# Optimization experiments

Hardware: AMD Instinct MI355X
Metric: run time of the kernel (lower is better)

## Reference

```python
import jax, jax.numpy as jnp
import numpy as np

WINDOW_SIZE = 256

def setup_inputs() -> dict:
    key = jax.random.key(0)
    kq, kk, kv = jax.random.split(key, 3)
    B, H, S, D = 1, 16, 4096, 64
    return {
        "query": jax.random.normal(kq, (B, H, S, D), dtype=jnp.float32),
        "key": jax.random.normal(kk, (B, H, S, D), dtype=jnp.float32),
        "value": jax.random.normal(kv, (B, H, S, D), dtype=jnp.float32),
    }

def reference(query, key, value):
    # Faithful to the torch module: dense QK^T, banded mask with -1e9 fill,
    # softmax over full row, then AV. Returns (output, attention_weights).
    d_k = query.shape[-1]
    S = query.shape[2]
    scores = jnp.einsum("bhqd,bhkd->bhqk", query, key) / jnp.sqrt(jnp.float32(d_k))
    idx = jnp.arange(S)
    band = jnp.abs(idx[:, None] - idx[None, :]) <= WINDOW_SIZE  # [S, S]
    scores = jnp.where(band[None, None, :, :], scores, jnp.float32(-1e9))
    attn = jax.nn.softmax(scores, axis=-1)
    out = jnp.einsum("bhqk,bhkd->bhqd", attn, value)
    return (out, attn)
```

## Files before the change

### kernel.cpp

```cpp
#include <hip/hip_runtime.h>
#include <math.h>

#define S_LEN 4096
#define D_DIM 64
#define H_NUM 16
#define WIN   256
#define TQ    32
#define NCH   9
#define KSTR  72
#define PBSTR 584

typedef __attribute__((ext_vector_type(8))) short          bf16x8;
typedef __attribute__((ext_vector_type(4))) float          f32x4;
typedef __attribute__((ext_vector_type(8))) unsigned short u16x8;
typedef __attribute__((ext_vector_type(4))) unsigned short u16x4;

static __device__ __forceinline__ unsigned short f2bf(float x) {
    unsigned int u = __float_as_uint(x);
    u = (u + 0x7FFFu + ((u >> 16) & 1u)) >> 16;
    return (unsigned short)u;
}
static __device__ __forceinline__ float bf2f(unsigned short h) {
    return __uint_as_float(((unsigned int)h) << 16);
}

__global__ __launch_bounds__(256) void swa_kernel(
    const float* __restrict__ Q,
    const float* __restrict__ K,
    const float* __restrict__ V,
    float* __restrict__ out,
    float* __restrict__ attn)
{
    const int tid = threadIdx.x;
    const int q0  = blockIdx.x * TQ;
    const int h   = blockIdx.y;

    const float* __restrict__ Qh = Q + (size_t)h * S_LEN * D_DIM;
    const float* __restrict__ Kh = K + (size_t)h * S_LEN * D_DIM;
    const float* __restrict__ Vh = V + (size_t)h * S_LEN * D_DIM;

    __shared__ unsigned short qbf[TQ * KSTR];
    __shared__ unsigned short kvb[64 * KSTR];
    __shared__ unsigned short pbf[TQ * PBSTR];
    __shared__ float red[4 * TQ];
    __shared__ float linv[TQ];

    const int k0   = max(q0 - WIN, 0);
    const int lane = tid & 63;
    const int wv   = tid >> 6;
    const int quad = lane >> 4;
    const int n16  = lane & 15;

    const int skey = tid >> 2, sd0 = (tid & 3) * 16;

    float4 kx0, kx1, kx2, kx3;
    {
        const int kg = min(k0 + skey, S_LEN - 1);
        const float4* s4 = (const float4*)(Kh + (size_t)kg * D_DIM + sd0);
        kx0 = s4[0]; kx1 = s4[1]; kx2 = s4[2]; kx3 = s4[3];
    }

    {
        const int row = tid >> 3, c8 = (tid & 7) * 8;
        const float4 v0 = *(const float4*)(Qh + (size_t)(q0 + row) * D_DIM + c8);
        const float4 v1 = *(const float4*)(Qh + (size_t)(q0 + row) * D_DIM + c8 + 4);
        u16x8 p;
        p[0]=f2bf(v0.x); p[1]=f2bf(v0.y); p[2]=f2bf(v0.z); p[3]=f2bf(v0.w);
        p[4]=f2bf(v1.x); p[5]=f2bf(v1.y); p[6]=f2bf(v1.z); p[7]=f2bf(v1.w);
        *(u16x8*)&qbf[row * KSTR + c8] = p;
    }
    __syncthreads();

    bf16x8 aqf[2][2];
    #pragma unroll
    for (int qt = 0; qt < 2; ++qt) {
        aqf[qt][0] = *(const bf16x8*)&qbf[(qt * 16 + n16) * KSTR + quad * 8];
        aqf[qt][1] = *(const bf16x8*)&qbf[(qt * 16 + n16) * KSTR + 32 + quad * 8];
    }

    float psum[8] = {0.f,0.f,0.f,0.f,0.f,0.f,0.f,0.f};
    #pragma unroll
    for (int c = 0; c < NCH; ++c) {
        const int kb = k0 + c * 64;
        {
            u16x8 p0, p1;
            p0[0]=f2bf(kx0.x); p0[1]=f2bf(kx0.y); p0[2]=f2bf(kx0.z); p0[3]=f2bf(kx0.w);
            p0[4]=f2bf(kx1.x); p0[5]=f2bf(kx1.y); p0[6]=f2bf(kx1.z); p0[7]=f2bf(kx1.w);
            p1[0]=f2bf(kx2.x); p1[1]=f2bf(kx2.y); p1[2]=f2bf(kx2.z); p1[3]=f2bf(kx2.w);
            p1[4]=f2bf(kx3.x); p1[5]=f2bf(kx3.y); p1[6]=f2bf(kx3.z); p1[7]=f2bf(kx3.w);
            *(u16x8*)&kvb[skey * KSTR + sd0]     = p0;
            *(u16x8*)&kvb[skey * KSTR + sd0 + 8] = p1;
        }
        __syncthreads();

        if (c + 1 < NCH) {
            const int kg = min(kb + 64 + skey, S_LEN - 1);
            const float4* s4 = (const float4*)(Kh + (size_t)kg * D_DIM + sd0);
            kx0 = s4[0]; kx1 = s4[1]; kx2 = s4[2]; kx3 = s4[3];
        }

        const bf16x8 b0 = *(const bf16x8*)&kvb[(wv * 16 + n16) * KSTR + quad * 8];
        const bf16x8 b1 = *(const bf16x8*)&kvb[(wv * 16 + n16) * KSTR + 32 + quad * 8];
        const int key_abs = kb + wv * 16 + n16;
        #pragma unroll
        for (int qt = 0; qt < 2; ++qt) {
            f32x4 acc = {0.f, 0.f, 0.f, 0.f};
            acc = __builtin_amdgcn_mfma_f32_16x16x32_bf16(aqf[qt][0], b0, acc, 0, 0, 0);
            acc = __builtin_amdgcn_mfma_f32_16x16x32_bf16(aqf[qt][1], b1, acc, 0, 0, 0);

            #pragma unroll
            for (int r = 0; r < 4; ++r) {
                const int qrow  = qt * 16 + quad * 4 + r;
                const int q_abs = q0 + qrow;
                const bool in   = (key_abs < S_LEN) &&
                                  (key_abs >= q_abs - WIN) && (key_abs <= q_abs + WIN);
                const float e = in ? __expf(acc[r] * 0.125f) : 0.f;
                pbf[qrow * PBSTR + c * 64 + wv * 16 + n16] = f2bf(e);
                psum[qt * 4 + r] += e;
            }
        }
        __syncthreads();
    }

    float4 vx0, vx1, vx2, vx3;
    {
        const int kg = min(k0 + skey, S_LEN - 1);
        const float4* s4 = (const float4*)(Vh + (size_t)kg * D_DIM + sd0);
        vx0 = s4[0]; vx1 = s4[1]; vx2 = s4[2]; vx3 = s4[3];
    }

    #pragma unroll
    for (int i = 0; i < 8; ++i) {
        float s = psum[i];
        s += __shfl_down(s, 8, 16);
        s += __shfl_down(s, 4, 16);
        s += __shfl_down(s, 2, 16);
        s += __shfl_down(s, 1, 16);
        if (n16 == 0) red[wv * TQ + (i >> 2) * 16 + quad * 4 + (i & 3)] = s;
    }
    __syncthreads();
    if (tid < TQ)
        linv[tid] = 1.f / (red[tid] + red[TQ + tid] + red[2 * TQ + tid] + red[3 * TQ + tid]);
    __syncthreads();

    f32x4 oacc0 = {0.f, 0.f, 0.f, 0.f};
    f32x4 oacc1 = {0.f, 0.f, 0.f, 0.f};
    const int dd = wv * 16 + n16;
    const int sd = ((dd >> 4) + (dd & 7)) & 7;
    #pragma unroll
    for (int c = 0; c < NCH; ++c) {
        {
            const float vals[16] = {vx0.x,vx0.y,vx0.z,vx0.w, vx1.x,vx1.y,vx1.z,vx1.w,
                                    vx2.x,vx2.y,vx2.z,vx2.w, vx3.x,vx3.y,vx3.z,vx3.w};
            #pragma unroll
            for (int jj = 0; jj < 16; ++jj) {
                const int d  = sd0 + jj;
                const int sw = ((d >> 4) + (d & 7)) & 7;
                kvb[d * 64 + (skey ^ (sw * 8))] = f2bf(vals[jj]);
            }
        }
        __syncthreads();

        if (c + 1 < NCH) {
            const int kg = min(k0 + (c + 1) * 64 + skey, S_LEN - 1);
            const float4* s4 = (const float4*)(Vh + (size_t)kg * D_DIM + sd0);
            vx0 = s4[0]; vx1 = s4[1]; vx2 = s4[2]; vx3 = s4[3];
        }

        const bf16x8 vb0 = *(const bf16x8*)&kvb[dd * 64 + 8 * (quad ^ sd)];
        const bf16x8 vb1 = *(const bf16x8*)&kvb[dd * 64 + 8 * ((4 + quad) ^ sd)];
        const bf16x8 pa00 = *(const bf16x8*)&pbf[n16 * PBSTR + c * 64 + quad * 8];
        const bf16x8 pa01 = *(const bf16x8*)&pbf[n16 * PBSTR + c * 64 + 32 + quad * 8];
        const bf16x8 pa10 = *(const bf16x8*)&pbf[(16 + n16) * PBSTR + c * 64 + quad * 8];
        const bf16x8 pa11 = *(const bf16x8*)&pbf[(16 + n16) * PBSTR + c * 64 + 32 + quad * 8];
        oacc0 = __builtin_amdgcn_mfma_f32_16x16x32_bf16(pa00, vb0, oacc0, 0, 0, 0);
        oacc0 = __builtin_amdgcn_mfma_f32_16x16x32_bf16(pa01, vb1, oacc0, 0, 0, 0);
        oacc1 = __builtin_amdgcn_mfma_f32_16x16x32_bf16(pa10, vb0, oacc1, 0, 0, 0);
        oacc1 = __builtin_amdgcn_mfma_f32_16x16x32_bf16(pa11, vb1, oacc1, 0, 0, 0);
        __syncthreads();
    }
    #pragma unroll
    for (int r = 0; r < 4; ++r) {
        const int qr = quad * 4 + r;
        out[((size_t)h * S_LEN + q0 + qr) * D_DIM + dd]      = oacc0[r] * linv[qr];
        out[((size_t)h * S_LEN + q0 + 16 + qr) * D_DIM + dd] = oacc1[r] * linv[16 + qr];
    }

    for (int qq = 0; qq < TQ; ++qq) {
        const int qa  = q0 + qq;
        const int b0q = max(qa - WIN, 0);
        const int b1q = min(qa + WIN, S_LEN - 1);
        const float qi = linv[qq];
        f32x4* arow = (f32x4*)(attn + ((size_t)h * S_LEN + qa) * S_LEN);
        const unsigned short* prow = &pbf[qq * PBSTR];
        for (int j4 = tid; j4 < S_LEN / 4; j4 += 256) {
            const int j = j4 * 4;
            f32x4 w = {0.f, 0.f, 0.f, 0.f};
            if (j >= b0q && j + 3 <= b1q) {
                const u16x4 p = *(const u16x4*)&prow[j - k0];
                w[0] = bf2f(p.x) * qi; w[1] = bf2f(p.y) * qi;
                w[2] = bf2f(p.z) * qi; w[3] = bf2f(p.w) * qi;
            } else if (j + 3 >= b0q && j <= b1q) {
                #pragma unroll
                for (int e = 0; e < 4; ++e) {
                    const int jj = j + e;
                    if (jj >= b0q && jj <= b1q) w[e] = bf2f(prow[jj - k0]) * qi;
                }
            }
            __builtin_nontemporal_store(w, &arow[j4]);
        }
    }
}

extern "C" void kernel_launch(void* const* d_in, const int* in_sizes, int n_in,
                              void* d_out, int out_size, void* d_ws, size_t ws_size,
                              hipStream_t stream) {
    const float* Q = (const float*)d_in[0];
    const float* K = (const float*)d_in[1];
    const float* V = (const float*)d_in[2];
    float* out  = (float*)d_out;
    float* attn = out + (size_t)H_NUM * S_LEN * D_DIM;

    dim3 grid(S_LEN / TQ, H_NUM);
    swa_kernel<<<grid, 256, 0, stream>>>(Q, K, V, out, attn);
}
```

Measured before the change: 1.126 ms.

## Interleave out-of-band attn zero stores with compute phases, write band region at end

The zero fill of the attention matrix outside each block's key window is now spread across the QK and PV chunk loops, two query rows per chunk, so the large store traffic overlaps MFMA and load work. The final epilogue writes only the 144 float4 columns covering the window, instead of sweeping all 4096 columns per row. This keeps the write-bandwidth-bound output streaming through the whole kernel rather than only at the tail, at the cost of extra instructions and register pressure inside the main loops.

```diff
diff --git a/kernel.cpp b/kernel.cpp
--- a/kernel.cpp
+++ b/kernel.cpp
@@ -51,6 +51,29 @@
     const int quad = lane >> 4;
     const int n16  = lane & 15;
 
+    const int l4  = k0 >> 2;
+    const int e4  = l4 + 144;
+    const int r4  = (e4 < 1024) ? (1024 - e4) : 0;
+    const int zp4 = l4 + r4;
+    const f32x4 zero4 = {0.f, 0.f, 0.f, 0.f};
+
+#define ZEROS(p)                                                                 \
+    if ((p) < 16) {                                                              \
+        _Pragma("unroll")                                                        \
+        for (int rr = 0; rr < 2; ++rr) {                                         \
+            const int qq = 2 * (p) + rr;                                         \
+            f32x4* arow = (f32x4*)(attn + ((size_t)h * S_LEN + q0 + qq) * S_LEN);\
+            _Pragma("unroll")                                                    \
+            for (int it = 0; it < 4; ++it) {                                     \
+                const int c4 = tid + it * 256;                                   \
+                if (c4 < zp4) {                                                  \
+                    const int col4 = (c4 < l4) ? c4 : (c4 - l4 + e4);            \
+                    __builtin_nontemporal_store(zero4, &arow[col4]);             \
+                }                                                                \
+            }                                                                    \
+        }                                                                        \
+    }
+
     const int skey = tid >> 2, sd0 = (tid & 3) * 16;
 
     float4 kx0, kx1, kx2, kx3;
@@ -93,6 +116,8 @@
         }
         __syncthreads();
 
+        ZEROS(c);
+
         if (c + 1 < NCH) {
             const int kg = min(kb + 64 + skey, S_LEN - 1);
             const float4* s4 = (const float4*)(Kh + (size_t)kg * D_DIM + sd0);
@@ -161,6 +186,8 @@
         }
         __syncthreads();
 
+        ZEROS(9 + c);
+
         if (c + 1 < NCH) {
             const int kg = min(k0 + (c + 1) * 64 + skey, S_LEN - 1);
             const float4* s4 = (const float4*)(Vh + (size_t)kg * D_DIM + sd0);
@@ -186,15 +213,17 @@
         out[((size_t)h * S_LEN + q0 + 16 + qr) * D_DIM + dd] = oacc1[r] * linv[16 + qr];
     }
 
-    for (int qq = 0; qq < TQ; ++qq) {
-        const int qa  = q0 + qq;
-        const int b0q = max(qa - WIN, 0);
-        const int b1q = min(qa + WIN, S_LEN - 1);
-        const float qi = linv[qq];
-        f32x4* arow = (f32x4*)(attn + ((size_t)h * S_LEN + qa) * S_LEN);
-        const unsigned short* prow = &pbf[qq * PBSTR];
-        for (int j4 = tid; j4 < S_LEN / 4; j4 += 256) {
-            const int j = j4 * 4;
+    for (int i = tid; i < TQ * 144; i += 256) {
+        const int qq   = i / 144;
+        const int c4   = i - qq * 144;
+        const int col4 = l4 + c4;
+        if (col4 < 1024) {
+            const int qa  = q0 + qq;
+            const int b0q = max(qa - WIN, 0);
+            const int b1q = min(qa + WIN, S_LEN - 1);
+            const float qi = linv[qq];
+            const unsigned short* prow = &pbf[qq * PBSTR];
+            const int j = col4 * 4;
             f32x4 w = {0.f, 0.f, 0.f, 0.f};
             if (j >= b0q && j + 3 <= b1q) {
                 const u16x4 p = *(const u16x4*)&prow[j - k0];
@@ -207,9 +236,11 @@
                     if (jj >= b0q && jj <= b1q) w[e] = bf2f(prow[jj - k0]) * qi;
                 }
             }
-            __builtin_nontemporal_store(w, &arow[j4]);
-        }
-    }
+            f32x4* arow = (f32x4*)(attn + ((size_t)h * S_LEN + qa) * S_LEN);
+            __builtin_nontemporal_store(w, &arow[col4]);
+        }
+    }
+#undef ZEROS
 }
 
 extern "C" void kernel_launch(void* const* d_in, const int* in_sizes, int n_in,
```

New measurement: 1.100 ms. -2.3%, faster.
